# Kernel tuning notes

Measured on AMD Instinct MI355X. Metric: run time of the kernel, lower is better.

The kernel has to match this reference:

```python
import jax, jax.numpy as jnp
import numpy as np

B, I, H = 4096, 1024, 1024


def setup_inputs() -> dict:
    key = jax.random.key(0)
    ks = jax.random.split(key, 7)
    s = 0.1  # matches uniform(-0.1, 0.1) init scale loosely
    return {
        "input": jax.random.normal(ks[0], (B, I), jnp.float32),
        "h_t": jax.random.normal(ks[1], (B, H), jnp.float32),
        "c_t": jax.random.normal(ks[2], (B, H), jnp.float32),
        "w_i": jax.random.uniform(ks[3], (I, 4 * H), jnp.float32, -s, s),
        "w_h": jax.random.uniform(ks[4], (H, 4 * H), jnp.float32, -s, s),
        "b_i": jax.random.uniform(ks[5], (4 * H,), jnp.float32, -s, s),
        "b_h": jax.random.uniform(ks[6], (4 * H,), jnp.float32, -s, s),
    }


def reference(input, h_t, c_t, w_i, w_h, b_i, b_h):
    # ifgo: [B, 4H] = x @ w_i + h @ w_h + b_i + b_h
    ifgo = input @ w_i + h_t @ w_h + (b_i + b_h)
    i, f, g, o = jnp.split(ifgo, 4, axis=1)
    i = jax.nn.sigmoid(i)
    f = jax.nn.sigmoid(f)
    g = jnp.tanh(g)
    o = jax.nn.sigmoid(o)
    c_new = f * c_t + i * g
    h_new = o * jnp.tanh(c_new)
    return (h_new, c_new)
```

## Files before the change

### kernel.cpp

```cpp
#include <hip/hip_runtime.h>
#include <stdint.h>

typedef __attribute__((ext_vector_type(8))) short short8;
typedef __attribute__((ext_vector_type(4))) float floatx4;

__device__ inline unsigned short f2bf(float x) {
  union { float f; unsigned int u; } v; v.f = x;
  unsigned int r = v.u + 0x7FFFu + ((v.u >> 16) & 1u);
  return (unsigned short)(r >> 16);
}

__global__ void pack_all(const float* __restrict__ x, const float* __restrict__ h,
                         const float* __restrict__ wi, const float* __restrict__ wh,
                         unsigned short* __restrict__ A,
                         unsigned short* __restrict__ Wt) {
  int bid = blockIdx.x;
  int t = threadIdx.x;
  if (bid < 4096) {
    int idx = bid * 256 + t;
    int row = idx >> 8;
    int kc  = (idx & 255) << 3;
    const float* src = (kc < 1024) ? (x + (size_t)row * 1024 + kc)
                                   : (h + (size_t)row * 1024 + (kc - 1024));
    float4 a = ((const float4*)src)[0];
    float4 b = ((const float4*)src)[1];
    uint4 o;
    o.x = f2bf(a.x) | ((unsigned)f2bf(a.y) << 16);
    o.y = f2bf(a.z) | ((unsigned)f2bf(a.w) << 16);
    o.z = f2bf(b.x) | ((unsigned)f2bf(b.y) << 16);
    o.w = f2bf(b.z) | ((unsigned)f2bf(b.w) << 16);
    *(uint4*)(A + (size_t)row * 2048 + kc) = o;
  } else {
    __shared__ float tile[64][65];
    int b2 = bid - 4096;
    int kt = b2 & 31;
    int nt = b2 >> 5;
    int k0 = kt << 6, n0 = nt << 6;
    const float* src = (k0 < 1024) ? (wi + (size_t)k0 * 4096)
                                   : (wh + (size_t)(k0 - 1024) * 4096);
    int c4 = (t & 15) << 2, rr = t >> 4;
#pragma unroll
    for (int p = 0; p < 4; ++p) {
      int kk = rr + p * 16;
      float4 v = *(const float4*)(src + (size_t)kk * 4096 + n0 + c4);
      tile[kk][c4 + 0] = v.x; tile[kk][c4 + 1] = v.y;
      tile[kk][c4 + 2] = v.z; tile[kk][c4 + 3] = v.w;
    }
    __syncthreads();
    int k8 = (t & 7) << 3, nn = t >> 3;
#pragma unroll
    for (int p = 0; p < 2; ++p) {
      int n = n0 + nn + p * 32;
      int hh = n & 1023, g = n >> 10;
      int R = ((hh >> 5) << 7) + (((hh >> 4) & 1) << 6) + (g << 4) + (hh & 15);
      int nl = nn + p * 32;
      uint4 o;
      o.x = f2bf(tile[k8 + 0][nl]) | ((unsigned)f2bf(tile[k8 + 1][nl]) << 16);
      o.y = f2bf(tile[k8 + 2][nl]) | ((unsigned)f2bf(tile[k8 + 3][nl]) << 16);
      o.z = f2bf(tile[k8 + 4][nl]) | ((unsigned)f2bf(tile[k8 + 5][nl]) << 16);
      o.w = f2bf(tile[k8 + 6][nl]) | ((unsigned)f2bf(tile[k8 + 7][nl]) << 16);
      *(uint4*)(Wt + (size_t)R * 2048 + k0 + k8) = o;
    }
  }
}

__device__ inline void gl_lds16(const void* g, void* l) {
  __builtin_amdgcn_global_load_lds(
      (const __attribute__((address_space(1))) void*)g,
      (__attribute__((address_space(3))) void*)l, 16, 0, 0);
}

__device__ inline float sigm(float x)  { return 1.0f / (1.0f + __expf(-x)); }
__device__ inline float tanhx(float x) { return 2.0f / (1.0f + __expf(-2.0f * x)) - 1.0f; }

__global__ void __launch_bounds__(256, 3) gemm_lstm(
    const unsigned short* __restrict__ A,
    const unsigned short* __restrict__ Bt,
    const float* __restrict__ ct,
    const float* __restrict__ bi,
    const float* __restrict__ bh,
    float* __restrict__ out) {
  constexpr int K = 2048;
  __shared__ char AsB[128 * 128];
  __shared__ char BsB[128 * 128];
  const int tid  = threadIdx.x;
  const int lane = tid & 63;
  const int wave = tid >> 6;
  const int wm = wave >> 1, wn = wave & 1;
  const int m0 = blockIdx.y << 7;
  const int n0 = blockIdx.x << 7;
  const int h0 = blockIdx.x << 5;

  const int er = (lane >> 4) << 2;
  const int ec = lane & 15;
  const int h  = h0 + (wn << 4) + ec;
  float bias[4];
#pragma unroll
  for (int j = 0; j < 4; ++j) bias[j] = bi[j * 1024 + h] + bh[j * 1024 + h];

  const int sr = tid >> 3;
  const int cs = ((tid & 7) ^ (sr & 7)) << 4;
  const unsigned voff = (unsigned)sr * 4096u + (unsigned)cs;
  const char* aBase = (const char*)A  + (size_t)m0 * 4096;
  const char* bBase = (const char*)Bt + (size_t)n0 * 4096;
  char* aD = AsB + tid * 16;
  char* bD = BsB + tid * 16;

  floatx4 acc[4][4] = {};
  const int rA = (wm << 6) + (lane & 15);
  const int rB = (wn << 6) + (lane & 15);
  const int keyc = lane & 7;
  const int kq   = lane >> 4;
  const char* aF0 = AsB + rA * 128 + ((kq ^ keyc) << 4);
  const char* aF1 = AsB + rA * 128 + (((4 + kq) ^ keyc) << 4);
  const char* bF0 = BsB + rB * 128 + ((kq ^ keyc) << 4);
  const char* bF1 = BsB + rB * 128 + (((4 + kq) ^ keyc) << 4);

  for (int ks = 0; ks < K; ks += 64) {
    const char* aIt = aBase + ks * 2;
    const char* bIt = bBase + ks * 2;
#pragma unroll
    for (int p = 0; p < 4; ++p) gl_lds16(aIt + p * 131072 + voff, aD + p * 4096);
#pragma unroll
    for (int p = 0; p < 4; ++p) gl_lds16(bIt + p * 131072 + voff, bD + p * 4096);
    __syncthreads();
    {
      short8 af[4], bfr[4];
#pragma unroll
      for (int f = 0; f < 4; ++f) {
        af[f]  = *(const short8*)(aF0 + f * 2048);
        bfr[f] = *(const short8*)(bF0 + f * 2048);
      }
#pragma unroll
      for (int i = 0; i < 4; ++i)
#pragma unroll
        for (int j = 0; j < 4; ++j)
          acc[i][j] = __builtin_amdgcn_mfma_f32_16x16x32_bf16(af[i], bfr[j], acc[i][j], 0, 0, 0);
    }
    {
      short8 af[4], bfr[4];
#pragma unroll
      for (int f = 0; f < 4; ++f) {
        af[f]  = *(const short8*)(aF1 + f * 2048);
        bfr[f] = *(const short8*)(bF1 + f * 2048);
      }
#pragma unroll
      for (int i = 0; i < 4; ++i)
#pragma unroll
        for (int j = 0; j < 4; ++j)
          acc[i][j] = __builtin_amdgcn_mfma_f32_16x16x32_bf16(af[i], bfr[j], acc[i][j], 0, 0, 0);
    }
    __syncthreads();
  }

  float cv[4][4];
#pragma unroll
  for (int i = 0; i < 4; ++i)
#pragma unroll
    for (int rg = 0; rg < 4; ++rg) {
      int row = m0 + (wm << 6) + i * 16 + er + rg;
      cv[i][rg] = ct[(size_t)row * 1024 + h];
    }
#pragma unroll
  for (int i = 0; i < 4; ++i) {
#pragma unroll
    for (int rg = 0; rg < 4; ++rg) {
      int row = m0 + (wm << 6) + i * 16 + er + rg;
      size_t o = (size_t)row * 1024 + h;
      float iv = sigm(acc[i][0][rg] + bias[0]);
      float fv = sigm(acc[i][1][rg] + bias[1]);
      float gv = tanhx(acc[i][2][rg] + bias[2]);
      float ov = sigm(acc[i][3][rg] + bias[3]);
      float cn = fv * cv[i][rg] + iv * gv;
      out[o] = ov * tanhx(cn);
      out[4194304 + o] = cn;
    }
  }
}

extern "C" void kernel_launch(void* const* d_in, const int* in_sizes, int n_in,
                              void* d_out, int out_size, void* d_ws, size_t ws_size,
                              hipStream_t stream) {
  const float* x  = (const float*)d_in[0];
  const float* ht = (const float*)d_in[1];
  const float* ct = (const float*)d_in[2];
  const float* wi = (const float*)d_in[3];
  const float* wh = (const float*)d_in[4];
  const float* bi = (const float*)d_in[5];
  const float* bh = (const float*)d_in[6];
  float* out = (float*)d_out;

  char* ws = (char*)d_ws;
  unsigned short* Abf = (unsigned short*)ws;
  unsigned short* Wbf = (unsigned short*)(ws + (16u << 20));

  pack_all<<<6144, 256, 0, stream>>>(x, ht, wi, wh, Abf, Wbf);
  gemm_lstm<<<dim3(32, 32), 256, 0, stream>>>(Abf, Wbf, ct, bi, bh, out);
}
```

Measured before the change: 197.7 us.

## Switch to 256x128 block tile with 32x32x16 bf16 MFMA and matching weight layout

The GEMM block tile grows from 128x128 to 256x128. Each wave now owns a 64-row by 128-column strip and uses 32x32x16 MFMA instructions instead of 16x16x32, and the packed weight row permutation changes to interleave gates in groups of 32 so each lane's four gate accumulators share the same hidden index. The goal is more reuse of each B tile across rows and fewer fragment loads per MFMA, lowering LDS and global traffic per flop. The costs are more LDS and accumulator registers, occupancy cut from 3 to 2 blocks per CU, and half as many blocks in the grid.

After: 198.4 us. About the same (+0.3%).

```diff
diff --git a/kernel.cpp b/kernel.cpp
--- a/kernel.cpp
+++ b/kernel.cpp
@@ -2,7 +2,7 @@
 #include <stdint.h>
 
 typedef __attribute__((ext_vector_type(8))) short short8;
-typedef __attribute__((ext_vector_type(4))) float floatx4;
+typedef __attribute__((ext_vector_type(16))) float floatx16;
 
 __device__ inline unsigned short f2bf(float x) {
   union { float f; unsigned int u; } v; v.f = x;
@@ -52,7 +52,7 @@
     for (int p = 0; p < 2; ++p) {
       int n = n0 + nn + p * 32;
       int hh = n & 1023, g = n >> 10;
-      int R = ((hh >> 5) << 7) + (((hh >> 4) & 1) << 6) + (g << 4) + (hh & 15);
+      int R = ((hh >> 5) << 7) + (g << 5) + (hh & 31);
       int nl = nn + p * 32;
       uint4 o;
       o.x = f2bf(tile[k8 + 0][nl]) | ((unsigned)f2bf(tile[k8 + 1][nl]) << 16);
@@ -73,7 +73,7 @@
 __device__ inline float sigm(float x)  { return 1.0f / (1.0f + __expf(-x)); }
 __device__ inline float tanhx(float x) { return 2.0f / (1.0f + __expf(-2.0f * x)) - 1.0f; }
 
-__global__ void __launch_bounds__(256, 3) gemm_lstm(
+__global__ void __launch_bounds__(256, 2) gemm_lstm(
     const unsigned short* __restrict__ A,
     const unsigned short* __restrict__ Bt,
     const float* __restrict__ ct,
@@ -81,19 +81,17 @@
     const float* __restrict__ bh,
     float* __restrict__ out) {
   constexpr int K = 2048;
-  __shared__ char AsB[128 * 128];
+  __shared__ char AsB[256 * 128];
   __shared__ char BsB[128 * 128];
   const int tid  = threadIdx.x;
   const int lane = tid & 63;
   const int wave = tid >> 6;
-  const int wm = wave >> 1, wn = wave & 1;
-  const int m0 = blockIdx.y << 7;
-  const int n0 = blockIdx.x << 7;
+  const int m0 = blockIdx.y << 8;
   const int h0 = blockIdx.x << 5;
 
-  const int er = (lane >> 4) << 2;
-  const int ec = lane & 15;
-  const int h  = h0 + (wn << 4) + ec;
+  const int el = lane & 31;
+  const int h5 = (lane >> 5) << 2;
+  const int h  = h0 + el;
   float bias[4];
 #pragma unroll
   for (int j = 0; j < 4; ++j) bias[j] = bi[j * 1024 + h] + bh[j * 1024 + h];
@@ -102,76 +100,64 @@
   const int cs = ((tid & 7) ^ (sr & 7)) << 4;
   const unsigned voff = (unsigned)sr * 4096u + (unsigned)cs;
   const char* aBase = (const char*)A  + (size_t)m0 * 4096;
-  const char* bBase = (const char*)Bt + (size_t)n0 * 4096;
+  const char* bBase = (const char*)Bt + (size_t)(blockIdx.x << 7) * 4096;
   char* aD = AsB + tid * 16;
   char* bD = BsB + tid * 16;
 
-  floatx4 acc[4][4] = {};
-  const int rA = (wm << 6) + (lane & 15);
-  const int rB = (wn << 6) + (lane & 15);
-  const int keyc = lane & 7;
-  const int kq   = lane >> 4;
-  const char* aF0 = AsB + rA * 128 + ((kq ^ keyc) << 4);
-  const char* aF1 = AsB + rA * 128 + (((4 + kq) ^ keyc) << 4);
-  const char* bF0 = BsB + rB * 128 + ((kq ^ keyc) << 4);
-  const char* bF1 = BsB + rB * 128 + (((4 + kq) ^ keyc) << 4);
+  floatx16 acc[2][4] = {};
+  const int lrow = lane & 31;
+  const int key  = lane & 7;
+  const int khalf = lane >> 5;
+  const char* aF = AsB + (wave * 64 + lrow) * 128;
+  const char* bF = BsB + lrow * 128;
+  int koff[4];
+#pragma unroll
+  for (int ks4 = 0; ks4 < 4; ++ks4) koff[ks4] = ((khalf + 2 * ks4) ^ key) << 4;
 
   for (int ks = 0; ks < K; ks += 64) {
     const char* aIt = aBase + ks * 2;
     const char* bIt = bBase + ks * 2;
 #pragma unroll
-    for (int p = 0; p < 4; ++p) gl_lds16(aIt + p * 131072 + voff, aD + p * 4096);
+    for (int p = 0; p < 8; ++p) gl_lds16(aIt + p * 131072 + voff, aD + p * 4096);
 #pragma unroll
     for (int p = 0; p < 4; ++p) gl_lds16(bIt + p * 131072 + voff, bD + p * 4096);
     __syncthreads();
-    {
-      short8 af[4], bfr[4];
 #pragma unroll
-      for (int f = 0; f < 4; ++f) {
-        af[f]  = *(const short8*)(aF0 + f * 2048);
-        bfr[f] = *(const short8*)(bF0 + f * 2048);
-      }
+    for (int kst = 0; kst < 4; ++kst) {
+      short8 af[2], bfr[4];
 #pragma unroll
-      for (int i = 0; i < 4; ++i)
+      for (int mb = 0; mb < 2; ++mb) af[mb] = *(const short8*)(aF + mb * 4096 + koff[kst]);
+#pragma unroll
+      for (int j = 0; j < 4; ++j)    bfr[j] = *(const short8*)(bF + j * 4096 + koff[kst]);
+#pragma unroll
+      for (int mb = 0; mb < 2; ++mb)
 #pragma unroll
         for (int j = 0; j < 4; ++j)
-          acc[i][j] = __builtin_amdgcn_mfma_f32_16x16x32_bf16(af[i], bfr[j], acc[i][j], 0, 0, 0);
-    }
-    {
-      short8 af[4], bfr[4];
-#pragma unroll
-      for (int f = 0; f < 4; ++f) {
-        af[f]  = *(const short8*)(aF1 + f * 2048);
-        bfr[f] = *(const short8*)(bF1 + f * 2048);
-      }
-#pragma unroll
-      for (int i = 0; i < 4; ++i)
-#pragma unroll
-        for (int j = 0; j < 4; ++j)
-          acc[i][j] = __builtin_amdgcn_mfma_f32_16x16x32_bf16(af[i], bfr[j], acc[i][j], 0, 0, 0);
+          acc[mb][j] = __builtin_amdgcn_mfma_f32_32x32x16_bf16(af[mb], bfr[j], acc[mb][j], 0, 0, 0);
     }
     __syncthreads();
   }
 
-  float cv[4][4];
+  const int rowbase = m0 + wave * 64 + h5;
+  float cv[2][16];
 #pragma unroll
-  for (int i = 0; i < 4; ++i)
+  for (int mb = 0; mb < 2; ++mb)
 #pragma unroll
-    for (int rg = 0; rg < 4; ++rg) {
-      int row = m0 + (wm << 6) + i * 16 + er + rg;
-      cv[i][rg] = ct[(size_t)row * 1024 + h];
+    for (int rg = 0; rg < 16; ++rg) {
+      int row = rowbase + mb * 32 + (rg & 3) + ((rg >> 2) << 3);
+      cv[mb][rg] = ct[(size_t)row * 1024 + h];
     }
 #pragma unroll
-  for (int i = 0; i < 4; ++i) {
+  for (int mb = 0; mb < 2; ++mb) {
 #pragma unroll
-    for (int rg = 0; rg < 4; ++rg) {
-      int row = m0 + (wm << 6) + i * 16 + er + rg;
+    for (int rg = 0; rg < 16; ++rg) {
+      int row = rowbase + mb * 32 + (rg & 3) + ((rg >> 2) << 3);
       size_t o = (size_t)row * 1024 + h;
-      float iv = sigm(acc[i][0][rg] + bias[0]);
-      float fv = sigm(acc[i][1][rg] + bias[1]);
-      float gv = tanhx(acc[i][2][rg] + bias[2]);
-      float ov = sigm(acc[i][3][rg] + bias[3]);
-      float cn = fv * cv[i][rg] + iv * gv;
+      float iv = sigm(acc[mb][0][rg] + bias[0]);
+      float fv = sigm(acc[mb][1][rg] + bias[1]);
+      float gv = tanhx(acc[mb][2][rg] + bias[2]);
+      float ov = sigm(acc[mb][3][rg] + bias[3]);
+      float cn = fv * cv[mb][rg] + iv * gv;
       out[o] = ov * tanhx(cn);
       out[4194304 + o] = cn;
     }
@@ -195,5 +181,5 @@
   unsigned short* Wbf = (unsigned short*)(ws + (16u << 20));
 
   pack_all<<<6144, 256, 0, stream>>>(x, ht, wi, wh, Abf, Wbf);
-  gemm_lstm<<<dim3(32, 32), 256, 0, stream>>>(Abf, Wbf, ct, bi, bh, out);
+  gemm_lstm<<<dim3(32, 16), 256, 0, stream>>>(Abf, Wbf, ct, bi, bh, out);
 }
```
